# Performance work log

Hardware: AMD Instinct MI355X
Metric: run time of the kernel (lower is better)

Reference implementation:

```python
import jax, jax.numpy as jnp
import numpy as np

THR = 1.0   # snntorch Leaky default threshold
BETA = 0.9  # leak factor from the module


@jax.custom_vjp
def atan_spike(x):
    # Heaviside forward; ATan surrogate gradient (snntorch default alpha=2):
    # d/dx = 1 / (1 + (pi * x)^2)
    return (x > 0).astype(x.dtype)

def _atan_fwd(x):
    return (x > 0).astype(x.dtype), x

def _atan_bwd(x, g):
    return (g / (1.0 + (jnp.pi * x) ** 2),)

atan_spike.defvjp(_atan_fwd, _atan_bwd)


def setup_inputs() -> dict:
    key = jax.random.key(0)
    k0, k1, k2, k3, k4 = jax.random.split(key, 5)
    B, T, L = 256, 1000, 30  # 24 = L - 7 + 1 matches fc1 in_features 16*24
    out_c = 35
    x = jax.random.normal(k0, (B, T, L), dtype=jnp.float32)
    conv_w = jax.random.normal(k1, (16, 1, 7), dtype=jnp.float32) / np.float32(np.sqrt(7.0))
    conv_b = jax.random.normal(k2, (16,), dtype=jnp.float32) * 0.05
    fc_w = jax.random.normal(k3, (out_c, 16 * 24), dtype=jnp.float32) / np.float32(np.sqrt(384.0))
    fc_b = jax.random.normal(k4, (out_c,), dtype=jnp.float32) * 0.05
    return {"x": x, "conv_w": conv_w, "conv_b": conv_b, "fc_w": fc_w, "fc_b": fc_b}


def reference(x, conv_w, conv_b, fc_w, fc_b):
    B, T, L = x.shape
    # Conv1d has no recurrence -> hoist it out of the time loop, batched over B*T.
    cur1 = jax.lax.conv_general_dilated(
        x.reshape(B * T, 1, L), conv_w, window_strides=(1,), padding="VALID",
        dimension_numbers=("NCH", "OIH", "NCH"),
    ) + conv_b[None, :, None]                      # (B*T, 16, 24)
    Lo = cur1.shape[-1]
    cur1 = cur1.reshape(B, T, 16, Lo).transpose(1, 0, 2, 3)  # (T, B, 16, 24)
    out_c = fc_w.shape[0]

    def step(carry, c1):
        mem1, mem2 = carry
        # LIF1: reset-by-subtraction using detached spike of previous membrane
        r1 = jax.lax.stop_gradient((mem1 > THR).astype(mem1.dtype))
        mem1 = BETA * mem1 + c1 - r1 * THR
        spk1 = atan_spike(mem1 - THR)              # (B, 16, 24)
        c2 = spk1.reshape(B, 16 * Lo) @ fc_w.T + fc_b  # (B, out_c)
        # LIF2
        r2 = jax.lax.stop_gradient((mem2 > THR).astype(mem2.dtype))
        mem2 = BETA * mem2 + c2 - r2 * THR
        return (mem1, mem2), mem2

    init = (jnp.zeros((B, 16, Lo), x.dtype), jnp.zeros((B, out_c), x.dtype))
    _, mem2_rec = jax.lax.scan(step, init, cur1)   # (T, B, out_c)
    return mem2_rec.mean(axis=0)                   # (B, out_c)
```

## Files before the change

### kernel.cpp

```cpp
#include <hip/hip_runtime.h>

typedef _Float16 half8 __attribute__((ext_vector_type(8)));
typedef float f32x4 __attribute__((ext_vector_type(4)));

#define SPH  32
#define NIT  34
#define SPKW 392
#define XTW  36
#define C2W  48
#define TN   1000


#define LOADBLK(BUF, S)                                                 \
    _Pragma("unroll")                                                   \
    for (int k = 0; k < 7; ++k)                                         \
        BUF[k] = *(const f32x4*)(xcol + k * XTW + (S));

#define CONV4(BUF, SB)                                                  \
    {                                                                   \
        float ca[4], cc[4];                                             \
        _Pragma("unroll")                                               \
        for (int dt = 0; dt < 4; ++dt) { ca[dt] = cb0; cc[dt] = cb1; }  \
        _Pragma("unroll")                                               \
        for (int k = 0; k < 7; ++k) {                                   \
            _Pragma("unroll")                                           \
            for (int dt = 0; dt < 4; ++dt) {                            \
                ca[dt] = fmaf(wk0[k], BUF[k][dt], ca[dt]);              \
                cc[dt] = fmaf(wk1[k], BUF[k][dt], cc[dt]);              \
            }                                                           \
        }                                                               \
        _Pragma("unroll")                                               \
        for (int dt = 0; dt < 4; ++dt) {                                \
            m1a = fmaf(0.9f, m1a, ca[dt] - spa);                        \
            spa = (m1a > 1.0f) ? 1.0f : 0.0f;                           \
            m1b = fmaf(0.9f, m1b, cc[dt] - spb);                        \
            spb = (m1b > 1.0f) ? 1.0f : 0.0f;                           \
            unsigned int pk = (m1a > 1.0f ? 0x00003C00u : 0u) |         \
                              (m1b > 1.0f ? 0x3C000000u : 0u);          \
            sdst[((SB) + dt) * (SPKW / 2)] = pk;                        \
        }                                                               \
    }

__global__ __launch_bounds__(576, 1) void snn_fwd(
    const float* __restrict__ x,
    const float* __restrict__ conv_w,
    const float* __restrict__ conv_b,
    const float* __restrict__ fc_w,
    const float* __restrict__ fc_b,
    float* __restrict__ out)
{
    __shared__ __align__(16) _Float16 spk[2][SPH][SPKW];
    __shared__ __align__(16) float    xsT[2][30][XTW];
    __shared__ __align__(16) float    c2L[2][SPH][C2W];

    const int tid  = threadIdx.x;
    const int b    = blockIdx.x;
    const int wid  = tid >> 6;
    const int lane = tid & 63;

    const int ct    = tid;
    const int cpair = ct & 7;
    const int p     = ct >> 3;
    const int c0    = cpair * 2;
    float wk0[7], wk1[7];
    float cb0 = 0.f, cb1 = 0.f;
    if (wid < 3) {
#pragma unroll
        for (int k = 0; k < 7; ++k) {
            wk0[k] = conv_w[c0 * 7 + k];
            wk1[k] = conv_w[(c0 + 1) * 7 + k];
        }
        cb0 = conv_b[c0];
        cb1 = conv_b[c0 + 1];
    }

    const int g  = wid - 3;
    const int m  = g >> 1;
    const int tb = g & 1;
    const int nL = lane & 15;
    const int q  = lane >> 4;
    half8 A[12];
    if (wid >= 3) {
        const int o = m * 16 + nL;
#pragma unroll
        for (int kt = 0; kt < 12; ++kt) {
            half8 a;
#pragma unroll
            for (int j = 0; j < 8; ++j) {
                int Kp = kt * 32 + q * 8 + j;
                int Kc = Kp & 15;
                int Kq = Kp >> 4;
                a[j] = (o < 35) ? (_Float16)fc_w[o * 384 + Kc * 24 + Kq]
                                : (_Float16)0.f;
            }
            A[kt] = a;
        }
    }
    const float fcb = (wid == 3 && lane < 35) ? fc_b[lane] : 0.f;

    const int st = tid - 192;
    int fs[3], fl[3];
    if (wid >= 3) {
#pragma unroll
        for (int r = 0; r < 3; ++r) {
            int f = st + 384 * r;
            fs[r] = f / 30;
            fl[r] = f % 30;
        }
    }

    float m1a = 0.f, spa = 0.f;
    float m1b = 0.f, spb = 0.f;
    float mem2 = 0.f, accO = 0.f;
    float xr[3];

    const float* xb = x + (size_t)b * (TN * 30);

    if (wid >= 3) {
#pragma unroll
        for (int r = 0; r < 3; ++r) {
            int f = st + 384 * r;
            if (f < 960) xsT[0][fl[r]][fs[r]] = xb[f];
        }
#pragma unroll
        for (int r = 0; r < 3; ++r) {
            int f = st + 384 * r;
            xr[r] = (f < 960) ? xb[960 + f] : 0.f;
        }
    }
    __syncthreads();

#pragma unroll 1
    for (int ph = 0; ph < NIT; ++ph) {
        if (wid < 3) {
            if (ph < 32) {
                const float* xcol = &xsT[ph & 1][p][0];
                unsigned int* sdst =
                    (unsigned int*)&spk[ph & 1][0][p * 16 + c0];

                f32x4 bufA[7], bufB[7];
                LOADBLK(bufA, 0)
#pragma unroll
                for (int blk = 0; blk < 8; blk += 2) {
                    LOADBLK(bufB, (blk + 1) * 4)
                    CONV4(bufA, blk * 4)
                    if (blk + 2 < 8) { LOADBLK(bufA, (blk + 2) * 4) }
                    CONV4(bufB, (blk + 1) * 4)
                }
            }
        } else {
            const bool ldg = (ph <= 29);
            float xn[3];
            if (ldg) {
                const float* src = xb + (size_t)(ph + 2) * (SPH * 30);
#pragma unroll
                for (int r = 0; r < 3; ++r) {
                    int f = st + 384 * r;
                    int t = (ph + 2) * SPH + fs[r];
                    xn[r] = (f < 960 && t < TN) ? src[f] : 0.f;
                }
            }
            if (ph >= 1 && ph <= 32) {
                const _Float16* sb = &spk[(ph - 1) & 1][0][0];
                half8 B[12];
#pragma unroll
                for (int kt = 0; kt < 12; ++kt)
                    B[kt] = *(const half8*)(sb + (tb * 16 + nL) * SPKW + kt * 32 + q * 8);
                f32x4 acc = {0.f, 0.f, 0.f, 0.f};
#pragma unroll
                for (int kt = 0; kt < 12; ++kt)
                    acc = __builtin_amdgcn_mfma_f32_16x16x32_f16(A[kt], B[kt], acc, 0, 0, 0);
                float* cd = &c2L[(ph - 1) & 1][0][0];
                *(f32x4*)(cd + (tb * 16 + nL) * C2W + m * 16 + q * 4) = acc;
            }
            if (wid == 3 && lane < 35 && ph >= 2) {
                const float* cs = &c2L[(ph - 2) & 1][0][0];
                float v[SPH];
#pragma unroll
                for (int j = 0; j < SPH; ++j) v[j] = cs[j * C2W + lane];
                const int tbase = (ph - 2) * SPH;
#pragma unroll
                for (int j = 0; j < SPH; ++j) {
                    float r2 = (mem2 > 1.0f) ? 1.0f : 0.0f;
                    mem2 = 0.9f * mem2 + (v[j] + fcb) - r2;
                    if (tbase + j < TN) accO += mem2;
                }
            }
            if (ph <= 30) {
                float* dst = &xsT[(ph + 1) & 1][0][0];
#pragma unroll
                for (int r = 0; r < 3; ++r) {
                    int f = st + 384 * r;
                    if (f < 960) dst[fl[r] * XTW + fs[r]] = xr[r];
                }
            }
            if (ldg) {
#pragma unroll
                for (int r = 0; r < 3; ++r) xr[r] = xn[r];
            }
        }
        __syncthreads();
    }

    if (wid == 3 && lane < 35) out[b * 35 + lane] = accO * (1.0f / (float)TN);
}

extern "C" void kernel_launch(void* const* d_in, const int* in_sizes, int n_in,
                              void* d_out, int out_size, void* d_ws, size_t ws_size,
                              hipStream_t stream) {
    const float* x      = (const float*)d_in[0];
    const float* conv_w = (const float*)d_in[1];
    const float* conv_b = (const float*)d_in[2];
    const float* fc_w   = (const float*)d_in[3];
    const float* fc_b   = (const float*)d_in[4];
    float* out          = (float*)d_out;

    snn_fwd<<<256, 576, 0, stream>>>(x, conv_w, conv_b, fc_w, fc_b, out);
}
```

Measured before the change: 146.3 us.

## Pack spike matrix as ballot bitmasks in LDS and expand to fp16 in MFMA warps

The conv/LIF1 warps now record spikes with wave ballots instead of writing one packed fp16 pair per thread per timestep. Each lane keeps one timestep's bitmask and the results go to a small bit array in shared memory. The channel mapping changes to cA and cA+8, so each ballot covers a whole half of the channels. The MFMA warps read a few 32-bit words per row and expand the bits into fp16 B operands with integer multiply and mask tricks. This removes most of the LDS stores and traffic for the spike matrix, at the cost of extra ALU work for the ballots, lane selects and bit expansion.

```diff
diff --git a/kernel.cpp b/kernel.cpp
--- a/kernel.cpp
+++ b/kernel.cpp
@@ -2,11 +2,14 @@
 
 typedef _Float16 half8 __attribute__((ext_vector_type(8)));
 typedef float f32x4 __attribute__((ext_vector_type(4)));
+typedef unsigned int uint;
+typedef uint uint2v __attribute__((ext_vector_type(2)));
+typedef uint uint4v __attribute__((ext_vector_type(4)));
 
 #define SPH  32
 #define NIT  34
-#define SPKW 392
 #define XTW  36
+#define BRW  12
 #define C2W  48
 #define TN   1000
 
@@ -16,7 +19,7 @@
     for (int k = 0; k < 7; ++k)                                         \
         BUF[k] = *(const f32x4*)(xcol + k * XTW + (S));
 
-#define CONV4(BUF, SB)                                                  \
+#define CONV4B(BUF, SB)                                                 \
     {                                                                   \
         float ca[4], cc[4];                                             \
         _Pragma("unroll")                                               \
@@ -35,9 +38,13 @@
             spa = (m1a > 1.0f) ? 1.0f : 0.0f;                           \
             m1b = fmaf(0.9f, m1b, cc[dt] - spb);                        \
             spb = (m1b > 1.0f) ? 1.0f : 0.0f;                           \
-            unsigned int pk = (m1a > 1.0f ? 0x00003C00u : 0u) |         \
-                              (m1b > 1.0f ? 0x3C000000u : 0u);          \
-            sdst[((SB) + dt) * (SPKW / 2)] = pk;                        \
+            unsigned long long Ab = __ballot(m1a > 1.0f);               \
+            unsigned long long Bb = __ballot(m1b > 1.0f);               \
+            const int ssel = (SB) + dt;                                 \
+            aLo = (lane == ssel) ? (uint)(Ab & 0xFFFFFFFFull) : aLo;    \
+            aHi = (lane == ssel) ? (uint)(Ab >> 32)           : aHi;    \
+            bLo = (lane == ssel) ? (uint)(Bb & 0xFFFFFFFFull) : bLo;    \
+            bHi = (lane == ssel) ? (uint)(Bb >> 32)           : bHi;    \
         }                                                               \
     }
 
@@ -49,29 +56,28 @@
     const float* __restrict__ fc_b,
     float* __restrict__ out)
 {
-    __shared__ __align__(16) _Float16 spk[2][SPH][SPKW];
-    __shared__ __align__(16) float    xsT[2][30][XTW];
-    __shared__ __align__(16) float    c2L[2][SPH][C2W];
+    __shared__ __align__(16) uint  bits[2][2][SPH][BRW];
+    __shared__ __align__(16) float xsT[2][30][XTW];
+    __shared__ __align__(16) float c2L[2][SPH][C2W];
 
     const int tid  = threadIdx.x;
     const int b    = blockIdx.x;
     const int wid  = tid >> 6;
     const int lane = tid & 63;
 
-    const int ct    = tid;
-    const int cpair = ct & 7;
-    const int p     = ct >> 3;
-    const int c0    = cpair * 2;
+    const int ct = tid;
+    const int cA = ct & 7;
+    const int p  = ct >> 3;
     float wk0[7], wk1[7];
     float cb0 = 0.f, cb1 = 0.f;
     if (wid < 3) {
 #pragma unroll
         for (int k = 0; k < 7; ++k) {
-            wk0[k] = conv_w[c0 * 7 + k];
-            wk1[k] = conv_w[(c0 + 1) * 7 + k];
-        }
-        cb0 = conv_b[c0];
-        cb1 = conv_b[c0 + 1];
+            wk0[k] = conv_w[cA * 7 + k];
+            wk1[k] = conv_w[(cA + 8) * 7 + k];
+        }
+        cb0 = conv_b[cA];
+        cb1 = conv_b[cA + 8];
     }
 
     const int g  = wid - 3;
@@ -135,17 +141,22 @@
         if (wid < 3) {
             if (ph < 32) {
                 const float* xcol = &xsT[ph & 1][p][0];
-                unsigned int* sdst =
-                    (unsigned int*)&spk[ph & 1][0][p * 16 + c0];
+                uint aLo = 0, aHi = 0, bLo = 0, bHi = 0;
 
                 f32x4 bufA[7], bufB[7];
                 LOADBLK(bufA, 0)
 #pragma unroll
                 for (int blk = 0; blk < 8; blk += 2) {
                     LOADBLK(bufB, (blk + 1) * 4)
-                    CONV4(bufA, blk * 4)
+                    CONV4B(bufA, blk * 4)
                     if (blk + 2 < 8) { LOADBLK(bufA, (blk + 2) * 4) }
-                    CONV4(bufB, (blk + 1) * 4)
+                    CONV4B(bufB, (blk + 1) * 4)
+                }
+                if (lane < 32) {
+                    uint2v va; va.x = aLo; va.y = aHi;
+                    uint2v vb; vb.x = bLo; vb.y = bHi;
+                    *(uint2v*)&bits[ph & 1][0][lane][wid * 2] = va;
+                    *(uint2v*)&bits[ph & 1][1][lane][wid * 2] = vb;
                 }
             }
         } else {
@@ -161,15 +172,27 @@
                 }
             }
             if (ph >= 1 && ph <= 32) {
-                const _Float16* sb = &spk[(ph - 1) & 1][0][0];
-                half8 B[12];
-#pragma unroll
-                for (int kt = 0; kt < 12; ++kt)
-                    B[kt] = *(const half8*)(sb + (tb * 16 + nL) * SPKW + kt * 32 + q * 8);
+                const int t = tb * 16 + nL;
+                const uint* bb = &bits[(ph - 1) & 1][q & 1][t][0];
+                uint4v dA = *(const uint4v*)bb;
+                uint2v dB = *(const uint2v*)(bb + 4);
+                uint d[6] = {dA.x, dA.y, dA.z, dA.w, dB.x, dB.y};
+                const uint qsh = (uint)((q >> 1) * 8);
                 f32x4 acc = {0.f, 0.f, 0.f, 0.f};
 #pragma unroll
-                for (int kt = 0; kt < 12; ++kt)
-                    acc = __builtin_amdgcn_mfma_f32_16x16x32_f16(A[kt], B[kt], acc, 0, 0, 0);
+                for (int kt = 0; kt < 12; ++kt) {
+                    uint mm = (d[kt >> 1] >> (qsh + 16 * (kt & 1))) & 0xFFu;
+                    uint sl  = ((mm & 0xFu) * 0x00204081u) & 0x01010101u;
+                    uint sh2 = (((mm >> 4) & 0xFu) * 0x00204081u) & 0x01010101u;
+                    uint slh = sl >> 16, shh = sh2 >> 16;
+                    uint w0 = (sl  & 1u) * 0x3C00u | (sl  & 0x100u) * 0x3C0000u;
+                    uint w1 = (slh & 1u) * 0x3C00u | (slh & 0x100u) * 0x3C0000u;
+                    uint w2 = (sh2 & 1u) * 0x3C00u | (sh2 & 0x100u) * 0x3C0000u;
+                    uint w3 = (shh & 1u) * 0x3C00u | (shh & 0x100u) * 0x3C0000u;
+                    uint4v wv; wv.x = w0; wv.y = w1; wv.z = w2; wv.w = w3;
+                    half8 Bf = __builtin_bit_cast(half8, wv);
+                    acc = __builtin_amdgcn_mfma_f32_16x16x32_f16(A[kt], Bf, acc, 0, 0, 0);
+                }
                 float* cd = &c2L[(ph - 1) & 1][0][0];
                 *(f32x4*)(cd + (tb * 16 + nL) * C2W + m * 16 + q * 4) = acc;
             }
```

Measured after the change: 226.2 us. 54.6% more time.

## Triple-buffer x tiles and prefetch next phase's conv inputs across barrier

Applied to the files above, without the earlier changes.

Expands the transposed x staging buffer from double to triple buffering so conv warps can preload the first blocks of the next phase's input before the barrier, keeping the register load pipeline running across phases. The global loader now runs one phase further ahead. It also raises the scheduling priority of the conv waves with s_setprio. The cost is extra shared memory, more live registers across the loop, and modulo-3 indexing.

```diff
diff --git a/kernel.cpp b/kernel.cpp
--- a/kernel.cpp
+++ b/kernel.cpp
@@ -15,6 +15,11 @@
     _Pragma("unroll")                                                   \
     for (int k = 0; k < 7; ++k)                                         \
         BUF[k] = *(const f32x4*)(xcol + k * XTW + (S));
+
+#define LOADBLKN(BUF, S)                                                \
+    _Pragma("unroll")                                                   \
+    for (int k = 0; k < 7; ++k)                                         \
+        BUF[k] = *(const f32x4*)(xcolN + k * XTW + (S));
 
 #define CONV4(BUF, SB)                                                  \
     {                                                                   \
@@ -50,7 +55,7 @@
     float* __restrict__ out)
 {
     __shared__ __align__(16) _Float16 spk[2][SPH][SPKW];
-    __shared__ __align__(16) float    xsT[2][30][XTW];
+    __shared__ __align__(16) float    xsT[3][30][XTW];
     __shared__ __align__(16) float    c2L[2][SPH][C2W];
 
     const int tid  = threadIdx.x;
@@ -65,6 +70,7 @@
     float wk0[7], wk1[7];
     float cb0 = 0.f, cb1 = 0.f;
     if (wid < 3) {
+        __builtin_amdgcn_s_setprio(1);
 #pragma unroll
         for (int k = 0; k < 7; ++k) {
             wk0[k] = conv_w[c0 * 7 + k];
@@ -113,50 +119,61 @@
     float m1b = 0.f, spb = 0.f;
     float mem2 = 0.f, accO = 0.f;
     float xr[3];
+    f32x4 bufA[7], bufB[7];
 
     const float* xb = x + (size_t)b * (TN * 30);
 
     if (wid >= 3) {
+#pragma unroll
+        for (int d = 0; d < 2; ++d) {
+#pragma unroll
+            for (int r = 0; r < 3; ++r) {
+                int f = st + 384 * r;
+                if (f < 960) xsT[d][fl[r]][fs[r]] = xb[d * 960 + f];
+            }
+        }
 #pragma unroll
         for (int r = 0; r < 3; ++r) {
             int f = st + 384 * r;
-            if (f < 960) xsT[0][fl[r]][fs[r]] = xb[f];
-        }
-#pragma unroll
-        for (int r = 0; r < 3; ++r) {
-            int f = st + 384 * r;
-            xr[r] = (f < 960) ? xb[960 + f] : 0.f;
+            xr[r] = (f < 960) ? xb[2 * 960 + f] : 0.f;
         }
     }
     __syncthreads();
+
+    if (wid < 3) {
+        const float* xcol = &xsT[0][p][0];
+        LOADBLK(bufA, 0)
+        LOADBLK(bufB, 4)
+    }
 
 #pragma unroll 1
     for (int ph = 0; ph < NIT; ++ph) {
         if (wid < 3) {
             if (ph < 32) {
-                const float* xcol = &xsT[ph & 1][p][0];
+                const float* xcol  = &xsT[ph % 3][p][0];
+                const float* xcolN = &xsT[(ph + 1) % 3][p][0];
                 unsigned int* sdst =
                     (unsigned int*)&spk[ph & 1][0][p * 16 + c0];
-
-                f32x4 bufA[7], bufB[7];
-                LOADBLK(bufA, 0)
-#pragma unroll
-                for (int blk = 0; blk < 8; blk += 2) {
-                    LOADBLK(bufB, (blk + 1) * 4)
-                    CONV4(bufA, blk * 4)
-                    if (blk + 2 < 8) { LOADBLK(bufA, (blk + 2) * 4) }
-                    CONV4(bufB, (blk + 1) * 4)
+#pragma unroll
+                for (int h = 0; h < 4; ++h) {
+                    const int blkA = 2 * h, blkB = 2 * h + 1;
+                    CONV4(bufA, blkA * 4)
+                    if (blkA + 2 < 8) { LOADBLK(bufA, (blkA + 2) * 4) }
+                    else              { LOADBLKN(bufA, (blkA - 6) * 4) }
+                    CONV4(bufB, blkB * 4)
+                    if (blkB + 2 < 8) { LOADBLK(bufB, (blkB + 2) * 4) }
+                    else              { LOADBLKN(bufB, (blkB - 6) * 4) }
                 }
             }
         } else {
-            const bool ldg = (ph <= 29);
+            const bool ldg = (ph <= 28);
             float xn[3];
             if (ldg) {
-                const float* src = xb + (size_t)(ph + 2) * (SPH * 30);
+                const float* src = xb + (size_t)(ph + 3) * (SPH * 30);
 #pragma unroll
                 for (int r = 0; r < 3; ++r) {
                     int f = st + 384 * r;
-                    int t = (ph + 2) * SPH + fs[r];
+                    int t = (ph + 3) * SPH + fs[r];
                     xn[r] = (f < 960 && t < TN) ? src[f] : 0.f;
                 }
             }
@@ -186,8 +203,8 @@
                     if (tbase + j < TN) accO += mem2;
                 }
             }
-            if (ph <= 30) {
-                float* dst = &xsT[(ph + 1) & 1][0][0];
+            if (ph <= 29) {
+                float* dst = &xsT[(ph + 2) % 3][0][0];
 #pragma unroll
                 for (int r = 0; r < 3; ++r) {
                     int f = st + 384 * r;
```

After: 150.2 us. 1.03x slower.

## Give each conv thread four channels and move LIF2 scan to dedicated wave

Applied to the files above, without the earlier changes.

The conv/LIF1 work drops from three waves (two channels per thread) to two waves (four channels per thread), so each loaded x column feeds four channels' FMAs and spikes go to LDS as 8-byte stores. The LIF2 time scan moves from an MFMA wave onto a separate ninth wave, taking it off the MFMA critical path. The x staging loop strides are adjusted for the new thread split. In exchange each conv thread does twice the serial LIF1 work per phase and holds more registers, which may lengthen the per-phase critical path.

```diff
diff --git a/kernel.cpp b/kernel.cpp
--- a/kernel.cpp
+++ b/kernel.cpp
@@ -2,6 +2,8 @@
 
 typedef _Float16 half8 __attribute__((ext_vector_type(8)));
 typedef float f32x4 __attribute__((ext_vector_type(4)));
+typedef unsigned int uint;
+typedef uint uint2v __attribute__((ext_vector_type(2)));
 
 #define SPH  32
 #define NIT  34
@@ -16,28 +18,38 @@
     for (int k = 0; k < 7; ++k)                                         \
         BUF[k] = *(const f32x4*)(xcol + k * XTW + (S));
 
-#define CONV4(BUF, SB)                                                  \
+#define CONV4Q(BUF, SB)                                                 \
     {                                                                   \
-        float ca[4], cc[4];                                             \
+        float ac[4][4];                                                 \
         _Pragma("unroll")                                               \
-        for (int dt = 0; dt < 4; ++dt) { ca[dt] = cb0; cc[dt] = cb1; }  \
+        for (int ci = 0; ci < 4; ++ci) {                                \
+            _Pragma("unroll")                                           \
+            for (int dt = 0; dt < 4; ++dt) ac[ci][dt] = cb[ci];         \
+        }                                                               \
         _Pragma("unroll")                                               \
         for (int k = 0; k < 7; ++k) {                                   \
             _Pragma("unroll")                                           \
-            for (int dt = 0; dt < 4; ++dt) {                            \
-                ca[dt] = fmaf(wk0[k], BUF[k][dt], ca[dt]);              \
-                cc[dt] = fmaf(wk1[k], BUF[k][dt], cc[dt]);              \
+            for (int ci = 0; ci < 4; ++ci) {                            \
+                _Pragma("unroll")                                       \
+                for (int dt = 0; dt < 4; ++dt)                          \
+                    ac[ci][dt] = fmaf(wk[ci][k], BUF[k][dt], ac[ci][dt]); \
             }                                                           \
         }                                                               \
         _Pragma("unroll")                                               \
         for (int dt = 0; dt < 4; ++dt) {                                \
-            m1a = fmaf(0.9f, m1a, ca[dt] - spa);                        \
-            spa = (m1a > 1.0f) ? 1.0f : 0.0f;                           \
-            m1b = fmaf(0.9f, m1b, cc[dt] - spb);                        \
-            spb = (m1b > 1.0f) ? 1.0f : 0.0f;                           \
-            unsigned int pk = (m1a > 1.0f ? 0x00003C00u : 0u) |         \
-                              (m1b > 1.0f ? 0x3C000000u : 0u);          \
-            sdst[((SB) + dt) * (SPKW / 2)] = pk;                        \
+            uint lo = 0u, hi = 0u;                                      \
+            _Pragma("unroll")                                           \
+            for (int ci = 0; ci < 4; ++ci) {                            \
+                m1[ci] = fmaf(0.9f, m1[ci], ac[ci][dt] - sp[ci]);       \
+                sp[ci] = (m1[ci] > 1.0f) ? 1.0f : 0.0f;                 \
+                uint bit = (m1[ci] > 1.0f) ? 0x3C00u : 0u;              \
+                if (ci == 0) lo |= bit;                                 \
+                if (ci == 1) lo |= bit << 16;                           \
+                if (ci == 2) hi |= bit;                                 \
+                if (ci == 3) hi |= bit << 16;                           \
+            }                                                           \
+            uint2v pk; pk.x = lo; pk.y = hi;                            \
+            *(uint2v*)(sdst + ((SB) + dt) * SPKW) = pk;                 \
         }                                                               \
     }
 
@@ -58,29 +70,29 @@
     const int wid  = tid >> 6;
     const int lane = tid & 63;
 
-    const int ct    = tid;
-    const int cpair = ct & 7;
-    const int p     = ct >> 3;
-    const int c0    = cpair * 2;
-    float wk0[7], wk1[7];
-    float cb0 = 0.f, cb1 = 0.f;
-    if (wid < 3) {
-#pragma unroll
-        for (int k = 0; k < 7; ++k) {
-            wk0[k] = conv_w[c0 * 7 + k];
-            wk1[k] = conv_w[(c0 + 1) * 7 + k];
-        }
-        cb0 = conv_b[c0];
-        cb1 = conv_b[c0 + 1];
-    }
-
-    const int g  = wid - 3;
+    const int ct = tid;
+    const int cq = ct & 3;
+    const int pr = ct >> 2;
+    const bool cvalid = (wid < 2) && (pr < 24);
+    const int p  = cvalid ? pr : 0;
+    float wk[4][7];
+    float cb[4];
+    if (wid < 2) {
+#pragma unroll
+        for (int ci = 0; ci < 4; ++ci) {
+#pragma unroll
+            for (int k = 0; k < 7; ++k) wk[ci][k] = conv_w[(cq * 4 + ci) * 7 + k];
+            cb[ci] = conv_b[cq * 4 + ci];
+        }
+    }
+
+    const int g  = wid - 2;
     const int m  = g >> 1;
     const int tb = g & 1;
     const int nL = lane & 15;
     const int q  = lane >> 4;
     half8 A[12];
-    if (wid >= 3) {
+    if (wid >= 2 && wid < 8) {
         const int o = m * 16 + nL;
 #pragma unroll
         for (int kt = 0; kt < 12; ++kt) {
@@ -96,35 +108,35 @@
             A[kt] = a;
         }
     }
-    const float fcb = (wid == 3 && lane < 35) ? fc_b[lane] : 0.f;
-
-    const int st = tid - 192;
+    const float fcb = (wid == 8 && lane < 35) ? fc_b[lane] : 0.f;
+
+    const int st = tid - 128;
     int fs[3], fl[3];
-    if (wid >= 3) {
+    if (wid >= 2) {
 #pragma unroll
         for (int r = 0; r < 3; ++r) {
-            int f = st + 384 * r;
+            int f = st + 448 * r;
             fs[r] = f / 30;
             fl[r] = f % 30;
         }
     }
 
-    float m1a = 0.f, spa = 0.f;
-    float m1b = 0.f, spb = 0.f;
+    float m1[4] = {0.f, 0.f, 0.f, 0.f};
+    float sp[4] = {0.f, 0.f, 0.f, 0.f};
     float mem2 = 0.f, accO = 0.f;
     float xr[3];
 
     const float* xb = x + (size_t)b * (TN * 30);
 
-    if (wid >= 3) {
+    if (wid >= 2) {
 #pragma unroll
         for (int r = 0; r < 3; ++r) {
-            int f = st + 384 * r;
+            int f = st + 448 * r;
             if (f < 960) xsT[0][fl[r]][fs[r]] = xb[f];
         }
 #pragma unroll
         for (int r = 0; r < 3; ++r) {
-            int f = st + 384 * r;
+            int f = st + 448 * r;
             xr[r] = (f < 960) ? xb[960 + f] : 0.f;
         }
     }
@@ -132,20 +144,19 @@
 
 #pragma unroll 1
     for (int ph = 0; ph < NIT; ++ph) {
-        if (wid < 3) {
-            if (ph < 32) {
+        if (wid < 2) {
+            if (ph < 32 && cvalid) {
                 const float* xcol = &xsT[ph & 1][p][0];
-                unsigned int* sdst =
-                    (unsigned int*)&spk[ph & 1][0][p * 16 + c0];
+                _Float16* sdst = &spk[ph & 1][0][p * 16 + cq * 4];
 
                 f32x4 bufA[7], bufB[7];
                 LOADBLK(bufA, 0)
 #pragma unroll
                 for (int blk = 0; blk < 8; blk += 2) {
                     LOADBLK(bufB, (blk + 1) * 4)
-                    CONV4(bufA, blk * 4)
+                    CONV4Q(bufA, blk * 4)
                     if (blk + 2 < 8) { LOADBLK(bufA, (blk + 2) * 4) }
-                    CONV4(bufB, (blk + 1) * 4)
+                    CONV4Q(bufB, (blk + 1) * 4)
                 }
             }
         } else {
@@ -155,12 +166,12 @@
                 const float* src = xb + (size_t)(ph + 2) * (SPH * 30);
 #pragma unroll
                 for (int r = 0; r < 3; ++r) {
-                    int f = st + 384 * r;
+                    int f = st + 448 * r;
                     int t = (ph + 2) * SPH + fs[r];
                     xn[r] = (f < 960 && t < TN) ? src[f] : 0.f;
                 }
             }
-            if (ph >= 1 && ph <= 32) {
+            if (wid < 8 && ph >= 1 && ph <= 32) {
                 const _Float16* sb = &spk[(ph - 1) & 1][0][0];
                 half8 B[12];
 #pragma unroll
@@ -173,7 +184,7 @@
                 float* cd = &c2L[(ph - 1) & 1][0][0];
                 *(f32x4*)(cd + (tb * 16 + nL) * C2W + m * 16 + q * 4) = acc;
             }
-            if (wid == 3 && lane < 35 && ph >= 2) {
+            if (wid == 8 && lane < 35 && ph >= 2) {
                 const float* cs = &c2L[(ph - 2) & 1][0][0];
                 float v[SPH];
 #pragma unroll
@@ -190,7 +201,7 @@
                 float* dst = &xsT[(ph + 1) & 1][0][0];
 #pragma unroll
                 for (int r = 0; r < 3; ++r) {
-                    int f = st + 384 * r;
+                    int f = st + 448 * r;
                     if (f < 960) dst[fl[r] * XTW + fs[r]] = xr[r];
                 }
             }
@@ -202,7 +213,7 @@
         __syncthreads();
     }
 
-    if (wid == 3 && lane < 35) out[b * 35 + lane] = accO * (1.0f / (float)TN);
+    if (wid == 8 && lane < 35) out[b * 35 + lane] = accO * (1.0f / (float)TN);
 }
 
 extern "C" void kernel_launch(void* const* d_in, const int* in_sizes, int n_in,
```

New measurement: 174.4 us. 19.2% more time.
